# Kernel tuning notes

Hardware: AMD Instinct MI355X
Metric: run time of the kernel (lower is better)

The kernel has to match this reference:

```python
import jax, jax.numpy as jnp
import numpy as np

B, L, H, D, VOC, C, P = 16, 256, 6, 768, 32000, 20, 1
d = D // H
MAXF = 20
BN_EPS = 1e-5


def setup_inputs() -> dict:
    key = jax.random.key(0)
    ks = jax.random.split(key, 8)
    doc_tids = jax.random.randint(ks[0], (B, L), 0, VOC)
    TFs = jax.random.uniform(ks[1], (B, L), dtype=jnp.float32) * 20.0 + 1.0
    DFs = jax.random.uniform(ks[2], (B, L), dtype=jnp.float32) * 1000.0 + 1.0
    emb = jax.random.normal(ks[3], (VOC, D), dtype=jnp.float32) * 0.02
    fcW = jax.random.normal(ks[4], (C + P, D), dtype=jnp.float32) * 0.02
    fcb = jnp.zeros((C + P,), dtype=jnp.float32)
    weiW = jax.random.normal(ks[5], (2, H), dtype=jnp.float32) * 0.1
    weib = jnp.zeros((2,), dtype=jnp.float32)
    return dict(doc_tids=doc_tids, TFs=TFs, DFs=DFs, emb=emb,
                fcW=fcW, fcb=fcb, weiW=weiW, weib=weib)


def _bn(x):
    # BatchNorm over channel axis 1 (H), batch stats over all other axes (train mode, affine=False)
    m = x.mean(axis=(0, 2, 3), keepdims=True)
    v = x.var(axis=(0, 2, 3), keepdims=True)
    return (x - m) * jax.lax.rsqrt(v + BN_EPS)


def _leaky9(x):
    return jnp.where(x >= 0, x, 9.0 * x)


def reference(doc_tids, TFs, DFs, emb, fcW, fcb, weiW, weib):
    # --- EmbbedingTFIDF (eval mode, dropout off): tf-idf weighted embedding lookup ---
    tf = jnp.minimum(TFs, float(MAXF))
    idf = jnp.log1p(1.0 / DFs)
    x = emb[doc_tids] * (tf * idf)[:, :, None]          # (B, L, D)
    valid = doc_tids != 0
    # model flips pad_mask with logical_not, then co_weights[pad_mask] = 0
    invalid = ~(valid[:, :, None] & valid[:, None, :])  # (B, L, L) True -> zero out
    mask = invalid[:, None, :, :]                       # broadcast over heads

    def split_heads(h):
        return h.reshape(B, L, H, d).transpose(0, 2, 1, 3)  # (B, H, L, d)

    Q = split_heads(x)
    K = Q
    V = Q

    # --- nearAttention (layers=1) ---
    Vn = _bn(V)
    # DistMatrix: pairwise Euclidean distance dist[b,h,i,j] = ||K_i - Q_j||
    Ksq = jnp.sum(K * K, axis=-1)[..., :, None]
    Qsq = jnp.sum(Q * Q, axis=-1)[..., None, :]
    cross = jnp.einsum('bhid,bhjd->bhij', K, Q)
    co = jnp.sqrt(jnp.maximum(Ksq + Qsq - 2.0 * cross, 1e-12))  # (B, H, L, L)
    # BatchNorm1d(H) over flattened (B, H, L*L) == per-H stats over (0,2,3)
    co = _leaky9(_bn(co))
    co = jnp.where(mask, 0.0, co)
    co = jax.nn.softmax(co, axis=-1)
    co = jnp.where(jnp.isnan(co), 0.0, co)
    V_out = jnp.einsum('bhij,bhjd->bhid', co, Vn)
    Q_out = _bn(jnp.einsum('bhij,bhjd->bhid', co, Q))
    K_out = _bn(jnp.einsum('bhij,bhjd->bhid', co, K))

    # --- head ---
    Vc = V_out.transpose(0, 2, 1, 3).reshape(B, L, D)       # catHiddens
    V_lgts = jax.nn.softmax(Vc @ fcW.T + fcb, axis=-1)      # (B, L, C+P)
    cw = jnp.swapaxes(co, -1, -2).reshape(B, L * L, H)      # transpose then contiguous reshape
    cw = jax.nn.softmax(cw @ weiW.T + weib, axis=-1)        # (B, L*L, 2)
    cw = cw.reshape(B, L, L, 2).sum(axis=-2, keepdims=True)[:, :, :, 0]  # (B, L, 1)
    cw = jax.nn.softmax(cw, axis=-1)                        # softmax over singleton -> ones (faithful)
    logits = (cw * V_lgts).sum(axis=1)[:, :C]               # (B, C)
    logits = jax.nn.softmax(logits, axis=-1)
    return logits
```

## Files before the change

kernel.cpp:

```cpp
#include <hip/hip_runtime.h>
#include <hip/hip_bf16.h>
#include <math.h>

#define OFF_XH   0UL
#define OFF_XT   1572864UL
#define OFF_CO   3145728UL
#define OFF_VC   6291456UL
#define OFF_SQ   7864320UL
#define OFF_THS  7888896UL
#define OFF_PART 7913472UL
#define OFF_STAT 7917000UL
#define OFF_ACC  7917024UL

typedef __attribute__((ext_vector_type(8))) __bf16 bf16x8;
typedef __attribute__((ext_vector_type(4))) float f32x4;
typedef __attribute__((ext_vector_type(8))) unsigned short u16x8;

__global__ __launch_bounds__(256) void k1_gather(const int* __restrict__ tids,
    const float* __restrict__ TF, const float* __restrict__ DF,
    const float* __restrict__ emb, unsigned short* __restrict__ xh,
    unsigned short* __restrict__ xT, float* __restrict__ sq, float* __restrict__ ths) {
  int bh = blockIdx.x >> 4, tg = blockIdx.x & 15;
  int b = bh / 6, h = bh % 6;
  int T0 = tg * 16;
  int tid = threadIdx.x;
  __shared__ float swgt[16];
  __shared__ int stid[16];
  __shared__ unsigned short tT[128][18];
  if (tid < 16) {
    int tok = b * 256 + T0 + tid;
    stid[tid] = tids[tok];
    swgt[tid] = fminf(TF[tok], 20.0f) * log1pf(1.0f / DF[tok]);
  }
  __syncthreads();
  int r = tid >> 4, c8 = (tid & 15) * 8;
  const float* er = emb + (size_t)stid[r] * 768 + h * 128 + c8;
  float wgt = swgt[r];
  float4 e0 = *(const float4*)er;
  float4 e1 = *(const float4*)(er + 4);
  float f[8] = {e0.x, e0.y, e0.z, e0.w, e1.x, e1.y, e1.z, e1.w};
  float s1 = 0.0f, s2 = 0.0f;
  u16x8 pk;
#pragma unroll
  for (int e = 0; e < 8; ++e) {
    __hip_bfloat16 hb = __float2bfloat16(f[e] * wgt);
    float g = __bfloat162float(hb);
    s1 += g; s2 += g * g;
    pk[e] = __bfloat16_as_ushort(hb);
  }
  *(u16x8*)(xh + ((size_t)(bh * 256 + T0 + r)) * 128 + c8) = pk;
  s1 += __shfl_down(s1, 8); s1 += __shfl_down(s1, 4);
  s1 += __shfl_down(s1, 2); s1 += __shfl_down(s1, 1);
  s2 += __shfl_down(s2, 8); s2 += __shfl_down(s2, 4);
  s2 += __shfl_down(s2, 2); s2 += __shfl_down(s2, 1);
  if ((tid & 15) == 0) {
    ths[bh * 256 + T0 + r] = s1;
    sq[bh * 256 + T0 + r]  = s2;
  }
#pragma unroll
  for (int j = 0; j < 8; ++j) tT[c8 + j][r] = pk[j];
  __syncthreads();
  int ch = tid >> 1, half = tid & 1;
  unsigned int* xo = (unsigned int*)xT + ((size_t)(bh * 128 + ch)) * 128 + tg * 8 + half * 4;
#pragma unroll
  for (int k = 0; k < 4; ++k)
    xo[k] = *(const unsigned int*)&tT[ch][(half * 4 + k) * 2];
}

__global__ __launch_bounds__(64) void k2_stats(const unsigned short* __restrict__ xh,
    const float* __restrict__ sq, float* __restrict__ part) {
  int p = blockIdx.x, bh = blockIdx.y;
  int lane = threadIdx.x;
  int quad = lane >> 4, l16 = lane & 15;
  int I = p * 16;
  const __bf16* xb = (const __bf16*)xh + (size_t)bh * 256 * 128;
  bf16x8 a[4];
#pragma unroll
  for (int k0 = 0; k0 < 4; ++k0)
    a[k0] = *(const bf16x8*)(xb + (size_t)(I + l16) * 128 + k0 * 32 + quad * 8);
  const float* sqh = sq + (size_t)bh * 256;
  float si[4];
#pragma unroll
  for (int r = 0; r < 4; ++r) si[r] = sqh[I + quad * 4 + r];
  float ls1 = 0.0f, ls2 = 0.0f;
#pragma unroll
  for (int t = 0; t < 16; ++t) {
    f32x4 acc = {0.0f, 0.0f, 0.0f, 0.0f};
#pragma unroll
    for (int k0 = 0; k0 < 4; ++k0) {
      bf16x8 bfr = *(const bf16x8*)(xb + (size_t)(t * 16 + l16) * 128 + k0 * 32 + quad * 8);
      acc = __builtin_amdgcn_mfma_f32_16x16x32_bf16(a[k0], bfr, acc, 0, 0, 0);
    }
    float sj = sqh[t * 16 + l16];
#pragma unroll
    for (int r = 0; r < 4; ++r) {
      float cv = sqrtf(fmaxf(si[r] + sj - 2.0f * acc[r], 1e-12f));
      ls1 += cv; ls2 += cv * cv;
    }
  }
#pragma unroll
  for (int off = 32; off >= 1; off >>= 1) {
    ls1 += __shfl_down(ls1, off);
    ls2 += __shfl_down(ls2, off);
  }
  if (lane == 0) {
    part[((size_t)bh * 16 + p) * 2 + 0] = ls1;
    part[((size_t)bh * 16 + p) * 2 + 1] = ls2;
  }
}

__global__ __launch_bounds__(384) void k3_stats(const float* __restrict__ ths,
    const float* __restrict__ sq, const float* __restrict__ part,
    float* __restrict__ stats, float* __restrict__ acc) {
  int h = threadIdx.x >> 6, lane = threadIdx.x & 63;
  float s1 = 0.0f, s2 = 0.0f;
  for (int m = 0; m < 64; ++m) {
    int f = m * 64 + lane;
    int bb = f >> 8, l = f & 255;
    size_t idx = ((size_t)(bb * 6 + h)) * 256 + l;
    s1 += ths[idx]; s2 += sq[idx];
  }
#pragma unroll
  for (int off = 32; off >= 1; off >>= 1) {
    s1 += __shfl_down(s1, off);
    s2 += __shfl_down(s2, off);
  }
  if (lane == 0) {
    float cnt = 524288.0f;
    float mean = s1 / cnt;
    float var = s2 / cnt - mean * mean;
    stats[h] = mean;
    stats[6 + h] = rsqrtf(var + 1e-5f);
  }
  float c1 = 0.0f, c2 = 0.0f;
#pragma unroll
  for (int t = 0; t < 4; ++t) {
    int e = lane + 64 * t;
    int bb = e >> 4, pp = e & 15;
    size_t pidx = ((size_t)(bb * 6 + h) * 16 + pp) * 2;
    c1 += part[pidx]; c2 += part[pidx + 1];
  }
#pragma unroll
  for (int off = 32; off >= 1; off >>= 1) {
    c1 += __shfl_down(c1, off);
    c2 += __shfl_down(c2, off);
  }
  if (lane == 0) {
    float cnt = 1048576.0f;
    float mean = c1 / cnt;
    float var = c2 / cnt - mean * mean;
    stats[12 + h] = mean;
    stats[18 + h] = rsqrtf(var + 1e-5f);
  }
  if (threadIdx.x < 336) acc[threadIdx.x] = 0.0f;
}

__global__ __launch_bounds__(64) void k4_fused(const unsigned short* __restrict__ xh,
    const int* __restrict__ tids, const float* __restrict__ sq,
    const float* __restrict__ stats, unsigned short* __restrict__ co16) {
  int p = blockIdx.x, bh = blockIdx.y;
  int b = bh / 6, h = bh % 6;
  int lane = threadIdx.x;
  int quad = lane >> 4, l16 = lane & 15;
  int I = p * 16;
  __shared__ float svld[256];
  __shared__ float ssq[256];
#pragma unroll
  for (int t = 0; t < 4; ++t) {
    int i = lane + 64 * t;
    svld[i] = (tids[b * 256 + i] != 0) ? 1.0f : 0.0f;
    ssq[i] = sq[(size_t)bh * 256 + i];
  }
  const __bf16* xb = (const __bf16*)xh + (size_t)bh * 256 * 128;
  bf16x8 a[4];
#pragma unroll
  for (int k0 = 0; k0 < 4; ++k0)
    a[k0] = *(const bf16x8*)(xb + (size_t)(I + l16) * 128 + k0 * 32 + quad * 8);
  __syncthreads();
  float m = stats[12 + h], rsc = stats[18 + h];
  float rv[4], si[4];
#pragma unroll
  for (int r = 0; r < 4; ++r) {
    rv[r] = svld[I + quad * 4 + r];
    si[r] = ssq[I + quad * 4 + r];
  }
  float y[16][4];
#pragma unroll
  for (int t = 0; t < 16; ++t) {
    f32x4 acc = {0.0f, 0.0f, 0.0f, 0.0f};
#pragma unroll
    for (int k0 = 0; k0 < 4; ++k0) {
      bf16x8 bfr = *(const bf16x8*)(xb + (size_t)(t * 16 + l16) * 128 + k0 * 32 + quad * 8);
      acc = __builtin_amdgcn_mfma_f32_16x16x32_bf16(a[k0], bfr, acc, 0, 0, 0);
    }
    float sj = ssq[t * 16 + l16];
    float cvld = svld[t * 16 + l16];
#pragma unroll
    for (int r = 0; r < 4; ++r) {
      float cv = sqrtf(fmaxf(si[r] + sj - 2.0f * acc[r], 1e-12f));
      float yv = (cv - m) * rsc;
      yv = yv >= 0.0f ? yv : 9.0f * yv;
      y[t][r] = yv * rv[r] * cvld;
    }
  }
  float inv[4];
#pragma unroll
  for (int r = 0; r < 4; ++r) {
    float mx = y[0][r];
#pragma unroll
    for (int t = 1; t < 16; ++t) mx = fmaxf(mx, y[t][r]);
#pragma unroll
    for (int off = 1; off <= 8; off <<= 1) mx = fmaxf(mx, __shfl_xor(mx, off));
    float s = 0.0f;
#pragma unroll
    for (int t = 0; t < 16; ++t) { y[t][r] = expf(y[t][r] - mx); s += y[t][r]; }
#pragma unroll
    for (int off = 1; off <= 8; off <<= 1) s += __shfl_xor(s, off);
    inv[r] = 1.0f / s;
  }
  size_t rowbase = ((size_t)bh * 256 + I + quad * 4) * 256;
#pragma unroll
  for (int t = 0; t < 16; ++t)
#pragma unroll
    for (int r = 0; r < 4; ++r)
      co16[rowbase + (size_t)r * 256 + t * 16 + l16] =
          __bfloat16_as_ushort(__float2bfloat16(y[t][r] * inv[r]));
}

__global__ __launch_bounds__(64) void k5a_vout(const unsigned short* __restrict__ co16,
    const unsigned short* __restrict__ xT, const float* __restrict__ stats,
    unsigned short* __restrict__ vc16) {
  int it = blockIdx.x;
  int bh = blockIdx.y;
  int b = bh / 6, h = bh % 6;
  int lane = threadIdx.x;
  int quad = lane >> 4, l16 = lane & 15;
  int I = it * 16;
  const __bf16* cb = (const __bf16*)co16 + ((size_t)(bh * 256 + I + l16)) * 256;
  bf16x8 a[8];
#pragma unroll
  for (int k0 = 0; k0 < 8; ++k0)
    a[k0] = *(const bf16x8*)(cb + k0 * 32 + quad * 8);
  const __bf16* xb = (const __bf16*)xT + (size_t)bh * 128 * 256;
  float m = stats[h], rs = stats[6 + h];
  float rm = rs * m;
  size_t vbase = ((size_t)(b * 256 + I + quad * 4)) * 768 + h * 128;
#pragma unroll
  for (int jt = 0; jt < 8; ++jt) {
    int ch = jt * 16 + l16;
    const __bf16* brow = xb + (size_t)ch * 256;
    f32x4 acc = {0.0f, 0.0f, 0.0f, 0.0f};
#pragma unroll
    for (int k0 = 0; k0 < 8; ++k0) {
      bf16x8 bfr = *(const bf16x8*)(brow + k0 * 32 + quad * 8);
      acc = __builtin_amdgcn_mfma_f32_16x16x32_bf16(a[k0], bfr, acc, 0, 0, 0);
    }
#pragma unroll
    for (int r = 0; r < 4; ++r) {
      float ov = rs * acc[r] - rm;
      vc16[vbase + (size_t)r * 768 + ch] = __bfloat16_as_ushort(__float2bfloat16(ov));
    }
  }
}

__global__ __launch_bounds__(256) void k5b_lgts(const unsigned short* __restrict__ vc16,
    const float* __restrict__ fcW, const float* __restrict__ fcb,
    float* __restrict__ acc) {
  int tid = threadIdx.x, w = tid >> 6, lane = tid & 63;
  int quad = lane >> 4, l16 = lane & 15;
  int tok0 = blockIdx.x * 64 + w * 16;
  int b = blockIdx.x >> 2;
  int c1c = (l16 < 5) ? (16 + l16) : 20;
  const __bf16* vb = (const __bf16*)vc16;
  const float* w0 = fcW + (size_t)l16 * 768;
  const float* w1 = fcW + (size_t)c1c * 768;
  f32x4 ac0 = {0.0f, 0.0f, 0.0f, 0.0f}, ac1 = {0.0f, 0.0f, 0.0f, 0.0f};
#pragma unroll
  for (int k0 = 0; k0 < 24; ++k0) {
    int ko = k0 * 32 + quad * 8;
    bf16x8 af = *(const bf16x8*)(vb + (size_t)(tok0 + l16) * 768 + ko);
    bf16x8 b0, b1;
#pragma unroll
    for (int e = 0; e < 8; ++e) {
      b0[e] = (__bf16)w0[ko + e];
      b1[e] = (__bf16)w1[ko + e];
    }
    ac0 = __builtin_amdgcn_mfma_f32_16x16x32_bf16(af, b0, ac0, 0, 0, 0);
    ac1 = __builtin_amdgcn_mfma_f32_16x16x32_bf16(af, b1, ac1, 0, 0, 0);
  }
  float bias0 = fcb[l16];
  float bias1 = (l16 < 5) ? fcb[16 + l16] : 0.0f;
  float p0s = 0.0f, p1s = 0.0f;
#pragma unroll
  for (int r = 0; r < 4; ++r) {
    float lg0 = ac0[r] + bias0;
    float lg1 = (l16 < 5) ? (ac1[r] + bias1) : -1e30f;
    float mx = fmaxf(lg0, lg1);
#pragma unroll
    for (int off = 1; off <= 8; off <<= 1) mx = fmaxf(mx, __shfl_xor(mx, off));
    float e0 = expf(lg0 - mx), e1 = expf(lg1 - mx);
    float s = e0 + e1;
#pragma unroll
    for (int off = 1; off <= 8; off <<= 1) s += __shfl_xor(s, off);
    float inv = 1.0f / s;
    p0s += e0 * inv;
    p1s += e1 * inv;
  }
  p0s += __shfl_xor(p0s, 16); p0s += __shfl_xor(p0s, 32);
  p1s += __shfl_xor(p1s, 16); p1s += __shfl_xor(p1s, 32);
  if (quad == 0) atomicAdd(&acc[b * 21 + l16], p0s);
  if (quad == 1 && l16 < 5) atomicAdd(&acc[b * 21 + 16 + l16], p1s);
}

__global__ __launch_bounds__(64) void k6_final(const float* __restrict__ acc,
                                               float* __restrict__ out) {
  int b = threadIdx.x;
  if (b < 16) {
    float mx = -1e30f;
    for (int c = 0; c < 20; ++c) mx = fmaxf(mx, acc[b * 21 + c]);
    float e[20], s = 0.0f;
    for (int c = 0; c < 20; ++c) { e[c] = expf(acc[b * 21 + c] - mx); s += e[c]; }
    float inv = 1.0f / s;
    for (int c = 0; c < 20; ++c) out[b * 20 + c] = e[c] * inv;
  }
}

extern "C" void kernel_launch(void* const* d_in, const int* in_sizes, int n_in,
                              void* d_out, int out_size, void* d_ws, size_t ws_size,
                              hipStream_t stream) {
  const int*   tids = (const int*)d_in[0];
  const float* TF   = (const float*)d_in[1];
  const float* DF   = (const float*)d_in[2];
  const float* emb  = (const float*)d_in[3];
  const float* fcW  = (const float*)d_in[4];
  const float* fcb  = (const float*)d_in[5];
  float* out = (float*)d_out;
  float* ws  = (float*)d_ws;
  unsigned short* xh = (unsigned short*)(ws + OFF_XH);
  unsigned short* xT = (unsigned short*)(ws + OFF_XT);
  unsigned short* co = (unsigned short*)(ws + OFF_CO);
  unsigned short* vc = (unsigned short*)(ws + OFF_VC);
  float* sq    = ws + OFF_SQ;
  float* ths   = ws + OFF_THS;
  float* part  = ws + OFF_PART;
  float* stats = ws + OFF_STAT;
  float* acc   = ws + OFF_ACC;

  k1_gather<<<1536, 256, 0, stream>>>(tids, TF, DF, emb, xh, xT, sq, ths);
  k2_stats<<<dim3(16, 96), 64, 0, stream>>>(xh, sq, part);
  k3_stats<<<1, 384, 0, stream>>>(ths, sq, part, stats, acc);
  k4_fused<<<dim3(16, 96), 64, 0, stream>>>(xh, tids, sq, stats, co);
  k5a_vout<<<dim3(16, 96), 64, 0, stream>>>(co, xT, stats, vc);
  k5b_lgts<<<64, 256, 0, stream>>>(vc, fcW, fcb, acc);
  k6_final<<<1, 64, 0, stream>>>(acc, out);
}
```

Measured before the change: 224.9 us.

## Fuse attention softmax with V-output matmul and merge logits with final softmax

The co-weight softmax tile is now written to shared memory and consumed directly by the V-output MFMA in the same block. This removes the global bf16 round trip of the full B×H×L×L attention matrix and one kernel launch. The logits kernel now runs one block per batch, reducing in shared memory and applying the final softmax in place. That removes the atomics, the accumulator zeroing and the last kernel launch, but leaves only 16 blocks to do the logits work.

```diff
diff --git a/kernel.cpp b/kernel.cpp
--- a/kernel.cpp
+++ b/kernel.cpp
@@ -4,13 +4,11 @@
 
 #define OFF_XH   0UL
 #define OFF_XT   1572864UL
-#define OFF_CO   3145728UL
-#define OFF_VC   6291456UL
-#define OFF_SQ   7864320UL
-#define OFF_THS  7888896UL
-#define OFF_PART 7913472UL
-#define OFF_STAT 7917000UL
-#define OFF_ACC  7917024UL
+#define OFF_VC   3145728UL
+#define OFF_SQ   4718592UL
+#define OFF_THS  4743168UL
+#define OFF_PART 4767744UL
+#define OFF_STAT 4770816UL
 
 typedef __attribute__((ext_vector_type(8))) __bf16 bf16x8;
 typedef __attribute__((ext_vector_type(4))) float f32x4;
@@ -111,7 +109,7 @@
 
 __global__ __launch_bounds__(384) void k3_stats(const float* __restrict__ ths,
     const float* __restrict__ sq, const float* __restrict__ part,
-    float* __restrict__ stats, float* __restrict__ acc) {
+    float* __restrict__ stats) {
   int h = threadIdx.x >> 6, lane = threadIdx.x & 63;
   float s1 = 0.0f, s2 = 0.0f;
   for (int m = 0; m < 64; ++m) {
@@ -152,12 +150,12 @@
     stats[12 + h] = mean;
     stats[18 + h] = rsqrtf(var + 1e-5f);
   }
-  if (threadIdx.x < 336) acc[threadIdx.x] = 0.0f;
-}
-
-__global__ __launch_bounds__(64) void k4_fused(const unsigned short* __restrict__ xh,
-    const int* __restrict__ tids, const float* __restrict__ sq,
-    const float* __restrict__ stats, unsigned short* __restrict__ co16) {
+}
+
+__global__ __launch_bounds__(64) void k45_fused(const unsigned short* __restrict__ xh,
+    const unsigned short* __restrict__ xT, const int* __restrict__ tids,
+    const float* __restrict__ sq, const float* __restrict__ stats,
+    unsigned short* __restrict__ vc16) {
   int p = blockIdx.x, bh = blockIdx.y;
   int b = bh / 6, h = bh % 6;
   int lane = threadIdx.x;
@@ -165,6 +163,7 @@
   int I = p * 16;
   __shared__ float svld[256];
   __shared__ float ssq[256];
+  __shared__ unsigned short cot[16][264];
 #pragma unroll
   for (int t = 0; t < 4; ++t) {
     int i = lane + 64 * t;
@@ -203,7 +202,6 @@
       y[t][r] = yv * rv[r] * cvld;
     }
   }
-  float inv[4];
 #pragma unroll
   for (int r = 0; r < 4; ++r) {
     float mx = y[0][r];
@@ -216,110 +214,98 @@
     for (int t = 0; t < 16; ++t) { y[t][r] = expf(y[t][r] - mx); s += y[t][r]; }
 #pragma unroll
     for (int off = 1; off <= 8; off <<= 1) s += __shfl_xor(s, off);
-    inv[r] = 1.0f / s;
-  }
-  size_t rowbase = ((size_t)bh * 256 + I + quad * 4) * 256;
-#pragma unroll
-  for (int t = 0; t < 16; ++t)
-#pragma unroll
-    for (int r = 0; r < 4; ++r)
-      co16[rowbase + (size_t)r * 256 + t * 16 + l16] =
-          __bfloat16_as_ushort(__float2bfloat16(y[t][r] * inv[r]));
-}
-
-__global__ __launch_bounds__(64) void k5a_vout(const unsigned short* __restrict__ co16,
-    const unsigned short* __restrict__ xT, const float* __restrict__ stats,
-    unsigned short* __restrict__ vc16) {
-  int it = blockIdx.x;
-  int bh = blockIdx.y;
-  int b = bh / 6, h = bh % 6;
-  int lane = threadIdx.x;
-  int quad = lane >> 4, l16 = lane & 15;
-  int I = it * 16;
-  const __bf16* cb = (const __bf16*)co16 + ((size_t)(bh * 256 + I + l16)) * 256;
-  bf16x8 a[8];
+    float inv = 1.0f / s;
+#pragma unroll
+    for (int t = 0; t < 16; ++t)
+      cot[quad * 4 + r][t * 16 + l16] =
+          __bfloat16_as_ushort(__float2bfloat16(y[t][r] * inv));
+  }
+  __syncthreads();
+  bf16x8 a2[8];
 #pragma unroll
   for (int k0 = 0; k0 < 8; ++k0)
-    a[k0] = *(const bf16x8*)(cb + k0 * 32 + quad * 8);
-  const __bf16* xb = (const __bf16*)xT + (size_t)bh * 128 * 256;
-  float m = stats[h], rs = stats[6 + h];
-  float rm = rs * m;
+    a2[k0] = *(const bf16x8*)&cot[l16][k0 * 32 + quad * 8];
+  const __bf16* xbT = (const __bf16*)xT + (size_t)bh * 128 * 256;
+  float mv = stats[h], rvs = stats[6 + h];
+  float rm = rvs * mv;
   size_t vbase = ((size_t)(b * 256 + I + quad * 4)) * 768 + h * 128;
 #pragma unroll
   for (int jt = 0; jt < 8; ++jt) {
     int ch = jt * 16 + l16;
-    const __bf16* brow = xb + (size_t)ch * 256;
-    f32x4 acc = {0.0f, 0.0f, 0.0f, 0.0f};
+    const __bf16* brow = xbT + (size_t)ch * 256;
+    f32x4 vacc = {0.0f, 0.0f, 0.0f, 0.0f};
 #pragma unroll
     for (int k0 = 0; k0 < 8; ++k0) {
       bf16x8 bfr = *(const bf16x8*)(brow + k0 * 32 + quad * 8);
-      acc = __builtin_amdgcn_mfma_f32_16x16x32_bf16(a[k0], bfr, acc, 0, 0, 0);
+      vacc = __builtin_amdgcn_mfma_f32_16x16x32_bf16(a2[k0], bfr, vacc, 0, 0, 0);
     }
 #pragma unroll
     for (int r = 0; r < 4; ++r) {
-      float ov = rs * acc[r] - rm;
+      float ov = rvs * vacc[r] - rm;
       vc16[vbase + (size_t)r * 768 + ch] = __bfloat16_as_ushort(__float2bfloat16(ov));
     }
   }
 }
 
-__global__ __launch_bounds__(256) void k5b_lgts(const unsigned short* __restrict__ vc16,
+__global__ __launch_bounds__(256) void k56_final(const unsigned short* __restrict__ vc16,
     const float* __restrict__ fcW, const float* __restrict__ fcb,
-    float* __restrict__ acc) {
+    float* __restrict__ out) {
+  int b = blockIdx.x;
   int tid = threadIdx.x, w = tid >> 6, lane = tid & 63;
   int quad = lane >> 4, l16 = lane & 15;
-  int tok0 = blockIdx.x * 64 + w * 16;
-  int b = blockIdx.x >> 2;
   int c1c = (l16 < 5) ? (16 + l16) : 20;
   const __bf16* vb = (const __bf16*)vc16;
   const float* w0 = fcW + (size_t)l16 * 768;
   const float* w1 = fcW + (size_t)c1c * 768;
-  f32x4 ac0 = {0.0f, 0.0f, 0.0f, 0.0f}, ac1 = {0.0f, 0.0f, 0.0f, 0.0f};
-#pragma unroll
-  for (int k0 = 0; k0 < 24; ++k0) {
-    int ko = k0 * 32 + quad * 8;
-    bf16x8 af = *(const bf16x8*)(vb + (size_t)(tok0 + l16) * 768 + ko);
-    bf16x8 b0, b1;
-#pragma unroll
-    for (int e = 0; e < 8; ++e) {
-      b0[e] = (__bf16)w0[ko + e];
-      b1[e] = (__bf16)w1[ko + e];
-    }
-    ac0 = __builtin_amdgcn_mfma_f32_16x16x32_bf16(af, b0, ac0, 0, 0, 0);
-    ac1 = __builtin_amdgcn_mfma_f32_16x16x32_bf16(af, b1, ac1, 0, 0, 0);
-  }
   float bias0 = fcb[l16];
   float bias1 = (l16 < 5) ? fcb[16 + l16] : 0.0f;
   float p0s = 0.0f, p1s = 0.0f;
-#pragma unroll
-  for (int r = 0; r < 4; ++r) {
-    float lg0 = ac0[r] + bias0;
-    float lg1 = (l16 < 5) ? (ac1[r] + bias1) : -1e30f;
-    float mx = fmaxf(lg0, lg1);
-#pragma unroll
-    for (int off = 1; off <= 8; off <<= 1) mx = fmaxf(mx, __shfl_xor(mx, off));
-    float e0 = expf(lg0 - mx), e1 = expf(lg1 - mx);
-    float s = e0 + e1;
-#pragma unroll
-    for (int off = 1; off <= 8; off <<= 1) s += __shfl_xor(s, off);
-    float inv = 1.0f / s;
-    p0s += e0 * inv;
-    p1s += e1 * inv;
+  for (int g = 0; g < 4; ++g) {
+    int tok0 = b * 256 + g * 64 + w * 16;
+    f32x4 ac0 = {0.0f, 0.0f, 0.0f, 0.0f}, ac1 = {0.0f, 0.0f, 0.0f, 0.0f};
+#pragma unroll
+    for (int k0 = 0; k0 < 24; ++k0) {
+      int ko = k0 * 32 + quad * 8;
+      bf16x8 af = *(const bf16x8*)(vb + (size_t)(tok0 + l16) * 768 + ko);
+      bf16x8 b0, b1;
+#pragma unroll
+      for (int e = 0; e < 8; ++e) {
+        b0[e] = (__bf16)w0[ko + e];
+        b1[e] = (__bf16)w1[ko + e];
+      }
+      ac0 = __builtin_amdgcn_mfma_f32_16x16x32_bf16(af, b0, ac0, 0, 0, 0);
+      ac1 = __builtin_amdgcn_mfma_f32_16x16x32_bf16(af, b1, ac1, 0, 0, 0);
+    }
+#pragma unroll
+    for (int r = 0; r < 4; ++r) {
+      float lg0 = ac0[r] + bias0;
+      float lg1 = (l16 < 5) ? (ac1[r] + bias1) : -1e30f;
+      float mx = fmaxf(lg0, lg1);
+#pragma unroll
+      for (int off = 1; off <= 8; off <<= 1) mx = fmaxf(mx, __shfl_xor(mx, off));
+      float e0 = expf(lg0 - mx), e1 = expf(lg1 - mx);
+      float s = e0 + e1;
+#pragma unroll
+      for (int off = 1; off <= 8; off <<= 1) s += __shfl_xor(s, off);
+      float inv = 1.0f / s;
+      p0s += e0 * inv;
+      p1s += e1 * inv;
+    }
   }
   p0s += __shfl_xor(p0s, 16); p0s += __shfl_xor(p0s, 32);
   p1s += __shfl_xor(p1s, 16); p1s += __shfl_xor(p1s, 32);
-  if (quad == 0) atomicAdd(&acc[b * 21 + l16], p0s);
-  if (quad == 1 && l16 < 5) atomicAdd(&acc[b * 21 + 16 + l16], p1s);
-}
-
-__global__ __launch_bounds__(64) void k6_final(const float* __restrict__ acc,
-                                               float* __restrict__ out) {
-  int b = threadIdx.x;
-  if (b < 16) {
+  __shared__ float sacc[4][21];
+  __shared__ float tot[21];
+  if (quad == 0) sacc[w][l16] = p0s;
+  if (quad == 1 && l16 < 5) sacc[w][16 + l16] = p1s;
+  __syncthreads();
+  if (tid < 21) tot[tid] = sacc[0][tid] + sacc[1][tid] + sacc[2][tid] + sacc[3][tid];
+  __syncthreads();
+  if (tid == 0) {
     float mx = -1e30f;
-    for (int c = 0; c < 20; ++c) mx = fmaxf(mx, acc[b * 21 + c]);
+    for (int c = 0; c < 20; ++c) mx = fmaxf(mx, tot[c]);
     float e[20], s = 0.0f;
-    for (int c = 0; c < 20; ++c) { e[c] = expf(acc[b * 21 + c] - mx); s += e[c]; }
+    for (int c = 0; c < 20; ++c) { e[c] = expf(tot[c] - mx); s += e[c]; }
     float inv = 1.0f / s;
     for (int c = 0; c < 20; ++c) out[b * 20 + c] = e[c] * inv;
   }
@@ -338,19 +324,15 @@
   float* ws  = (float*)d_ws;
   unsigned short* xh = (unsigned short*)(ws + OFF_XH);
   unsigned short* xT = (unsigned short*)(ws + OFF_XT);
-  unsigned short* co = (unsigned short*)(ws + OFF_CO);
   unsigned short* vc = (unsigned short*)(ws + OFF_VC);
   float* sq    = ws + OFF_SQ;
   float* ths   = ws + OFF_THS;
   float* part  = ws + OFF_PART;
   float* stats = ws + OFF_STAT;
-  float* acc   = ws + OFF_ACC;
 
   k1_gather<<<1536, 256, 0, stream>>>(tids, TF, DF, emb, xh, xT, sq, ths);
   k2_stats<<<dim3(16, 96), 64, 0, stream>>>(xh, sq, part);
-  k3_stats<<<1, 384, 0, stream>>>(ths, sq, part, stats, acc);
-  k4_fused<<<dim3(16, 96), 64, 0, stream>>>(xh, tids, sq, stats, co);
-  k5a_vout<<<dim3(16, 96), 64, 0, stream>>>(co, xT, stats, vc);
-  k5b_lgts<<<64, 256, 0, stream>>>(vc, fcW, fcb, acc);
-  k6_final<<<1, 64, 0, stream>>>(acc, out);
-}
+  k3_stats<<<1, 384, 0, stream>>>(ths, sq, part, stats);
+  k45_fused<<<dim3(16, 96), 64, 0, stream>>>(xh, xT, tids, sq, stats, vc);
+  k56_final<<<16, 256, 0, stream>>>(vc, fcW, fcb, out);
+}
```

Result: slower. 230.3 us (+2.4%).
